# Kernel tuning notes

Measured on AMD Instinct MI355X. Metric: run time of the kernel, lower is better.

## Reference

```python
import jax, jax.numpy as jnp
import numpy as np


def _conv3d(x, w):
    # x: [N, C, D, H, W], w: [O, C, 3, 3, 3], stride 1, padding 1 (same)
    return jax.lax.conv_general_dilated(
        x, w, window_strides=(1, 1, 1),
        padding=((1, 1), (1, 1), (1, 1)),
        dimension_numbers=('NCDHW', 'OIDHW', 'NCDHW'))


def setup_inputs() -> dict:
    key = jax.random.key(0)
    k1, k2, k3 = jax.random.split(key, 3)
    # x: [B, C, c_dim, time_steps, depth, H, W]
    x = jax.random.normal(k1, (2, 4, 8, 8, 8, 96, 96), dtype=jnp.float32)
    # 9 Conv3d kernels: index i*3+j = (c-offset i, t-offset j)
    W = jax.random.normal(k2, (9, 4, 4, 3, 3, 3), dtype=jnp.float32) * 0.1
    b = jax.random.normal(k3, (9, 4), dtype=jnp.float32) * 0.1
    return {'x': x, 'W': W, 'b': b}


def reference(x, W, b):
    # Conv5d(Conv4d(Conv3d)) with kernel=3, stride=1, padding=1.
    # out[:, :, c, t] = (1/9) * sum_{i,j in 0..2} Conv3d_{i,j}(x[:, :, c+i, t+j])
    # (inner /3 for the t-average times outer /3 for the c-average).
    B, C, cd, T, D, H, Wd = x.shape
    O = W.shape[1]
    Cc, Tt = cd - 2, T - 2  # valid c and t output positions
    acc = None
    for i in range(3):
        for j in range(3):
            # all (c, t) output windows at offset (i, j), fused into the batch dim
            xs = x[:, :, i:i + Cc, j:j + Tt]              # [B, C, Cc, Tt, D, H, W]
            xs = jnp.transpose(xs, (0, 2, 3, 1, 4, 5, 6))  # [B, Cc, Tt, C, D, H, W]
            xs = xs.reshape(B * Cc * Tt, C, D, H, Wd)
            y = _conv3d(xs, W[i * 3 + j])                  # [B*Cc*Tt, O, D, H, W]
            acc = y if acc is None else acc + y
    mean_bias = jnp.sum(b, axis=0) / 9.0                   # average of the 9 biases
    out = acc / 9.0 + mean_bias[None, :, None, None, None]
    out = out.reshape(B, Cc, Tt, O, D, H, Wd)
    return jnp.transpose(out, (0, 3, 1, 2, 4, 5, 6))       # [B, O, Cc, Tt, D, H, W]
```

## Files before the change

### kernel.cpp

```cpp
#include <hip/hip_runtime.h>


#define BLOCK 256
#define XSTRIDE 106

__global__ void prep_kernel(const float* __restrict__ Wg,
                            const float* __restrict__ bg,
                            float* __restrict__ ws)
{
    int k = blockIdx.x * blockDim.x + threadIdx.x;
    if (k < 3888) {
        int o  = k & 3;  int r = k >> 2;
        int kw = r % 3;  r /= 3;
        int kh = r % 3;  r /= 3;
        int kd = r % 3;  r /= 3;
        int ij = r % 9;  int ci = r / 9;
        ws[k] = Wg[ij*432 + o*108 + ci*27 + kd*9 + kh*3 + kw];
    }
    if (k < 4) {
        float s = 0.f;
        #pragma unroll
        for (int ij = 0; ij < 9; ++ij) s += bg[ij*4 + k];
        ws[3888 + k] = s * (1.0f / 9.0f);
    }
}

__global__ __launch_bounds__(256, 4) void conv5d_kernel(
    const float* __restrict__ xg,
    const float* __restrict__ wsW,
    float* __restrict__ outg)
{
    __shared__ float xs[54 * XSTRIDE];

    for (int k = threadIdx.x; k < 54 * XSTRIDE; k += BLOCK) xs[k] = 0.f;

    int bi   = blockIdx.x;
    int xcd  = bi & 7;
    int g    = bi >> 3;
    int slab = xcd*9 + g/48;
    int r2   = g % 48;
    int d    = r2 / 6;
    int ht   = r2 % 6;
    int b    = slab / 36;
    int ct   = slab % 36;
    int c    = ct / 6;
    int t    = ct % 6;
    int h0   = ht * 16;

    int wt     = threadIdx.x & 15;
    int hr_out = threadIdx.x >> 4;

    int  goff[6];
    int  lw[6];
    bool pv[6];
    #pragma unroll
    for (int p = 0; p < 6; ++p) {
        int u   = threadIdx.x + p*BLOCK;
        int row = u / 24;
        int q   = u % 24;
        int pl  = row / 18;
        int hr  = row % 18;
        int dd  = d + pl - 1;
        int hh  = h0 + hr - 1;
        pv[p]   = (u < 1296) && ((unsigned)dd < 8u) && ((unsigned)hh < 96u);
        goff[p] = dd*9216 + hh*96 + q*4;
        lw[p]   = row*XSTRIDE + 5 + q*4;
    }

    float acc[4][6] = {};

    #pragma unroll 1
    for (int it = 0; it < 36; ++it) {
        int ci = it / 9;
        int ij = it % 9;
        int i  = ij / 3;
        int j  = ij % 3;
        const float* xp = xg + (size_t)b*18874368 + (size_t)ci*4718592
                             + (size_t)(c + i)*589824
                             + (size_t)(t + j)*73728;

        __syncthreads();

        float4 v[6];
        #pragma unroll
        for (int p = 0; p < 6; ++p)
            if (pv[p]) v[p] = *(const float4*)(xp + goff[p]);
        #pragma unroll
        for (int p = 0; p < 6; ++p) {
            if (pv[p]) {
                xs[lw[p] + 0] = v[p].x;
                xs[lw[p] + 1] = v[p].y;
                xs[lw[p] + 2] = v[p].z;
                xs[lw[p] + 3] = v[p].w;
            }
        }
        __syncthreads();

        const float4* wq4 = (const float4*)(wsW + (ci*9 + ij)*108);
        #pragma unroll
        for (int pl = 0; pl < 3; ++pl) {
            #pragma unroll
            for (int kh = 0; kh < 3; ++kh) {
                const float2* xr2 = (const float2*)
                    &xs[(pl*18 + hr_out + kh)*XSTRIDE + 4 + 6*wt];
                float2 p0 = xr2[0], p1 = xr2[1], p2 = xr2[2], p3 = xr2[3];
                float xv[8] = {p0.x, p0.y, p1.x, p1.y, p2.x, p2.y, p3.x, p3.y};
                const float4* wr = wq4 + (pl*3 + kh)*3;
                float4 wk0 = wr[0];
                float4 wk1 = wr[1];
                float4 wk2 = wr[2];
                #pragma unroll
                for (int vv = 0; vv < 6; ++vv) {
                    float a = xv[vv], bb = xv[vv+1], cc = xv[vv+2];
                    acc[0][vv] = fmaf(a,  wk0.x, acc[0][vv]);
                    acc[1][vv] = fmaf(a,  wk0.y, acc[1][vv]);
                    acc[2][vv] = fmaf(a,  wk0.z, acc[2][vv]);
                    acc[3][vv] = fmaf(a,  wk0.w, acc[3][vv]);
                    acc[0][vv] = fmaf(bb, wk1.x, acc[0][vv]);
                    acc[1][vv] = fmaf(bb, wk1.y, acc[1][vv]);
                    acc[2][vv] = fmaf(bb, wk1.z, acc[2][vv]);
                    acc[3][vv] = fmaf(bb, wk1.w, acc[3][vv]);
                    acc[0][vv] = fmaf(cc, wk2.x, acc[0][vv]);
                    acc[1][vv] = fmaf(cc, wk2.y, acc[1][vv]);
                    acc[2][vv] = fmaf(cc, wk2.z, acc[2][vv]);
                    acc[3][vv] = fmaf(cc, wk2.w, acc[3][vv]);
                }
            }
        }
    }

    float4 mb4 = *(const float4*)(wsW + 3888);
    float mb[4] = {mb4.x, mb4.y, mb4.z, mb4.w};

    const float inv9 = 1.0f / 9.0f;
    size_t obase = (size_t)b*10616832 + (size_t)c*442368 + (size_t)t*73728
                 + (size_t)d*9216 + (size_t)(h0 + hr_out)*96 + 6*wt;
    #pragma unroll
    for (int o = 0; o < 4; ++o) {
        float* op = outg + obase + (size_t)o*2654208;
        #pragma unroll
        for (int vv = 0; vv < 3; ++vv) {
            float2 st;
            st.x = acc[o][2*vv]   * inv9 + mb[o];
            st.y = acc[o][2*vv+1] * inv9 + mb[o];
            *(float2*)(op + 2*vv) = st;
        }
    }
}

extern "C" void kernel_launch(void* const* d_in, const int* in_sizes, int n_in,
                              void* d_out, int out_size, void* d_ws, size_t ws_size,
                              hipStream_t stream) {
    const float* x = (const float*)d_in[0];
    const float* W = (const float*)d_in[1];
    const float* b = (const float*)d_in[2];
    float* out = (float*)d_out;
    float* ws  = (float*)d_ws;

    prep_kernel<<<16, BLOCK, 0, stream>>>(W, b, ws);
    conv5d_kernel<<<3456, BLOCK, 0, stream>>>(x, ws, out);
}
```

Baseline: 685.0 us.

## Compute two depth planes per block to reuse staged input planes

Each block now produces two adjacent output depth planes instead of one. It stages four input depth planes in shared memory rather than three, so input loads per output drop from 3 to 2 planes and the grid halves. The cost is more shared memory per block (72 rows vs 54), double the accumulator registers, and fewer blocks, which may lower occupancy.

```diff
diff --git a/kernel.cpp b/kernel.cpp
--- a/kernel.cpp
+++ b/kernel.cpp
@@ -30,44 +30,44 @@
     const float* __restrict__ wsW,
     float* __restrict__ outg)
 {
-    __shared__ float xs[54 * XSTRIDE];
+    __shared__ float xs[72 * XSTRIDE];
 
-    for (int k = threadIdx.x; k < 54 * XSTRIDE; k += BLOCK) xs[k] = 0.f;
+    for (int k = threadIdx.x; k < 72 * XSTRIDE; k += BLOCK) xs[k] = 0.f;
 
     int bi   = blockIdx.x;
     int xcd  = bi & 7;
     int g    = bi >> 3;
-    int slab = xcd*9 + g/48;
-    int r2   = g % 48;
-    int d    = r2 / 6;
+    int slab = xcd*9 + g/24;
+    int r2   = g % 24;
+    int dp   = r2 / 6;
     int ht   = r2 % 6;
     int b    = slab / 36;
     int ct   = slab % 36;
     int c    = ct / 6;
     int t    = ct % 6;
     int h0   = ht * 16;
+    int d0   = dp * 2;
 
     int wt     = threadIdx.x & 15;
     int hr_out = threadIdx.x >> 4;
 
-    int  goff[6];
-    int  lw[6];
-    bool pv[6];
+    int goff[7];
+    int lw[7];
     #pragma unroll
-    for (int p = 0; p < 6; ++p) {
+    for (int p = 0; p < 7; ++p) {
         int u   = threadIdx.x + p*BLOCK;
         int row = u / 24;
         int q   = u % 24;
         int pl  = row / 18;
         int hr  = row % 18;
-        int dd  = d + pl - 1;
+        int dd  = d0 + pl - 1;
         int hh  = h0 + hr - 1;
-        pv[p]   = (u < 1296) && ((unsigned)dd < 8u) && ((unsigned)hh < 96u);
-        goff[p] = dd*9216 + hh*96 + q*4;
+        bool ok = (u < 1728) && ((unsigned)dd < 8u) && ((unsigned)hh < 96u);
+        goff[p] = ok ? (dd*9216 + hh*96 + q*4) : -1;
         lw[p]   = row*XSTRIDE + 5 + q*4;
     }
 
-    float acc[4][6] = {};
+    float acc[2][4][6] = {};
 
     #pragma unroll 1
     for (int it = 0; it < 36; ++it) {
@@ -81,13 +81,13 @@
 
         __syncthreads();
 
-        float4 v[6];
+        float4 v[7];
         #pragma unroll
-        for (int p = 0; p < 6; ++p)
-            if (pv[p]) v[p] = *(const float4*)(xp + goff[p]);
+        for (int p = 0; p < 7; ++p)
+            if (goff[p] >= 0) v[p] = *(const float4*)(xp + goff[p]);
         #pragma unroll
-        for (int p = 0; p < 6; ++p) {
-            if (pv[p]) {
+        for (int p = 0; p < 7; ++p) {
+            if (goff[p] >= 0) {
                 xs[lw[p] + 0] = v[p].x;
                 xs[lw[p] + 1] = v[p].y;
                 xs[lw[p] + 2] = v[p].z;
@@ -98,32 +98,37 @@
 
         const float4* wq4 = (const float4*)(wsW + (ci*9 + ij)*108);
         #pragma unroll
-        for (int pl = 0; pl < 3; ++pl) {
+        for (int pl4 = 0; pl4 < 4; ++pl4) {
             #pragma unroll
             for (int kh = 0; kh < 3; ++kh) {
                 const float2* xr2 = (const float2*)
-                    &xs[(pl*18 + hr_out + kh)*XSTRIDE + 4 + 6*wt];
+                    &xs[(pl4*18 + hr_out + kh)*XSTRIDE + 4 + 6*wt];
                 float2 p0 = xr2[0], p1 = xr2[1], p2 = xr2[2], p3 = xr2[3];
                 float xv[8] = {p0.x, p0.y, p1.x, p1.y, p2.x, p2.y, p3.x, p3.y};
-                const float4* wr = wq4 + (pl*3 + kh)*3;
-                float4 wk0 = wr[0];
-                float4 wk1 = wr[1];
-                float4 wk2 = wr[2];
                 #pragma unroll
-                for (int vv = 0; vv < 6; ++vv) {
-                    float a = xv[vv], bb = xv[vv+1], cc = xv[vv+2];
-                    acc[0][vv] = fmaf(a,  wk0.x, acc[0][vv]);
-                    acc[1][vv] = fmaf(a,  wk0.y, acc[1][vv]);
-                    acc[2][vv] = fmaf(a,  wk0.z, acc[2][vv]);
-                    acc[3][vv] = fmaf(a,  wk0.w, acc[3][vv]);
-                    acc[0][vv] = fmaf(bb, wk1.x, acc[0][vv]);
-                    acc[1][vv] = fmaf(bb, wk1.y, acc[1][vv]);
-                    acc[2][vv] = fmaf(bb, wk1.z, acc[2][vv]);
-                    acc[3][vv] = fmaf(bb, wk1.w, acc[3][vv]);
-                    acc[0][vv] = fmaf(cc, wk2.x, acc[0][vv]);
-                    acc[1][vv] = fmaf(cc, wk2.y, acc[1][vv]);
-                    acc[2][vv] = fmaf(cc, wk2.z, acc[2][vv]);
-                    acc[3][vv] = fmaf(cc, wk2.w, acc[3][vv]);
+                for (int s = 0; s < 2; ++s) {
+                    int rel = pl4 - s;
+                    if (rel < 0 || rel > 2) continue;
+                    const float4* wr = wq4 + (rel*3 + kh)*3;
+                    float4 wk0 = wr[0];
+                    float4 wk1 = wr[1];
+                    float4 wk2 = wr[2];
+                    #pragma unroll
+                    for (int vv = 0; vv < 6; ++vv) {
+                        float a = xv[vv], bb = xv[vv+1], cc = xv[vv+2];
+                        acc[s][0][vv] = fmaf(a,  wk0.x, acc[s][0][vv]);
+                        acc[s][1][vv] = fmaf(a,  wk0.y, acc[s][1][vv]);
+                        acc[s][2][vv] = fmaf(a,  wk0.z, acc[s][2][vv]);
+                        acc[s][3][vv] = fmaf(a,  wk0.w, acc[s][3][vv]);
+                        acc[s][0][vv] = fmaf(bb, wk1.x, acc[s][0][vv]);
+                        acc[s][1][vv] = fmaf(bb, wk1.y, acc[s][1][vv]);
+                        acc[s][2][vv] = fmaf(bb, wk1.z, acc[s][2][vv]);
+                        acc[s][3][vv] = fmaf(bb, wk1.w, acc[s][3][vv]);
+                        acc[s][0][vv] = fmaf(cc, wk2.x, acc[s][0][vv]);
+                        acc[s][1][vv] = fmaf(cc, wk2.y, acc[s][1][vv]);
+                        acc[s][2][vv] = fmaf(cc, wk2.z, acc[s][2][vv]);
+                        acc[s][3][vv] = fmaf(cc, wk2.w, acc[s][3][vv]);
+                    }
                 }
             }
         }
@@ -133,17 +138,20 @@
     float mb[4] = {mb4.x, mb4.y, mb4.z, mb4.w};
 
     const float inv9 = 1.0f / 9.0f;
-    size_t obase = (size_t)b*10616832 + (size_t)c*442368 + (size_t)t*73728
-                 + (size_t)d*9216 + (size_t)(h0 + hr_out)*96 + 6*wt;
     #pragma unroll
-    for (int o = 0; o < 4; ++o) {
-        float* op = outg + obase + (size_t)o*2654208;
+    for (int s = 0; s < 2; ++s) {
+        size_t obase = (size_t)b*10616832 + (size_t)c*442368 + (size_t)t*73728
+                     + (size_t)(d0 + s)*9216 + (size_t)(h0 + hr_out)*96 + 6*wt;
         #pragma unroll
-        for (int vv = 0; vv < 3; ++vv) {
-            float2 st;
-            st.x = acc[o][2*vv]   * inv9 + mb[o];
-            st.y = acc[o][2*vv+1] * inv9 + mb[o];
-            *(float2*)(op + 2*vv) = st;
+        for (int o = 0; o < 4; ++o) {
+            float* op = outg + obase + (size_t)o*2654208;
+            #pragma unroll
+            for (int vv = 0; vv < 3; ++vv) {
+                float2 st;
+                st.x = acc[s][o][2*vv]   * inv9 + mb[o];
+                st.y = acc[s][o][2*vv+1] * inv9 + mb[o];
+                *(float2*)(op + 2*vv) = st;
+            }
         }
     }
 }
@@ -158,5 +166,5 @@
     float* ws  = (float*)d_ws;
 
     prep_kernel<<<16, BLOCK, 0, stream>>>(W, b, ws);
-    conv5d_kernel<<<3456, BLOCK, 0, stream>>>(x, ws, out);
+    conv5d_kernel<<<1728, BLOCK, 0, stream>>>(x, ws, out);
 }
```

Result: slower. 1.146 ms (+67.3%).
